# Kernel optimization log

Hardware: AMD Instinct MI355X
Metric: run time of the kernel (lower is better)

Reference implementation:

```python
import jax, jax.numpy as jnp
import numpy as np

DIM = 768
HEADS = 12
HD = DIM // HEADS
B, NX, NY = 8, 1024, 1024
GRID = 32
FREQ = 100.0
MLP_HID = 4 * DIM
EPS = 1e-5


def _grid_pos(batch, n, grid):
    g = int(np.sqrt(n))
    yy, xx = jnp.meshgrid(jnp.arange(g, dtype=jnp.int32), jnp.arange(g, dtype=jnp.int32), indexing='ij')
    pos = jnp.stack([yy.reshape(-1), xx.reshape(-1)], axis=-1)  # [N,2]
    return jnp.broadcast_to(pos[None], (batch, n, 2))


def setup_inputs() -> dict:
    key = jax.random.key(0)
    ks = jax.random.split(key, 16)
    s = 0.02
    inp = {
        'x': jax.random.normal(ks[0], (B, NX, DIM), jnp.float32),
        'y': jax.random.normal(ks[1], (B, NY, DIM), jnp.float32),
        'xpos': _grid_pos(B, NX, GRID),
        'ypos': _grid_pos(B, NY, GRID),
        # norms (gamma, beta)
        'norm1_g': jnp.ones((DIM,), jnp.float32), 'norm1_b': jnp.zeros((DIM,), jnp.float32),
        'norm2_g': jnp.ones((DIM,), jnp.float32), 'norm2_b': jnp.zeros((DIM,), jnp.float32),
        'norm3_g': jnp.ones((DIM,), jnp.float32), 'norm3_b': jnp.zeros((DIM,), jnp.float32),
        'normy_g': jnp.ones((DIM,), jnp.float32), 'normy_b': jnp.zeros((DIM,), jnp.float32),
        # self-attn: fused qkv (no bias, qkv_bias=False), out proj (with bias)
        'qkv_w': jax.random.normal(ks[2], (DIM, 3 * DIM), jnp.float32) * s,
        'attn_proj_w': jax.random.normal(ks[3], (DIM, DIM), jnp.float32) * s,
        'attn_proj_b': jnp.zeros((DIM,), jnp.float32),
        # cross-attn: separate q/k/v (no bias), out proj (with bias)
        'projq_w': jax.random.normal(ks[4], (DIM, DIM), jnp.float32) * s,
        'projk_w': jax.random.normal(ks[5], (DIM, DIM), jnp.float32) * s,
        'projv_w': jax.random.normal(ks[6], (DIM, DIM), jnp.float32) * s,
        'cross_proj_w': jax.random.normal(ks[7], (DIM, DIM), jnp.float32) * s,
        'cross_proj_b': jnp.zeros((DIM,), jnp.float32),
        # MLP
        'fc1_w': jax.random.normal(ks[8], (DIM, MLP_HID), jnp.float32) * s,
        'fc1_b': jnp.zeros((MLP_HID,), jnp.float32),
        'fc2_w': jax.random.normal(ks[9], (MLP_HID, DIM), jnp.float32) * s,
        'fc2_b': jnp.zeros((DIM,), jnp.float32),
    }
    return inp


def layernorm(x, g, b):
    m = jnp.mean(x, axis=-1, keepdims=True)
    v = jnp.mean(jnp.square(x - m), axis=-1, keepdims=True)
    return (x - m) * jax.lax.rsqrt(v + EPS) * g + b


def rope1d(tok, pos):
    # tok: [B,H,N,D], pos: [B,N] int
    D = tok.shape[-1]
    inv = 1.0 / (FREQ ** (jnp.arange(0, D, 2, dtype=jnp.float32) / D))  # [D/2]
    f = pos[:, None, :, None].astype(jnp.float32) * inv  # [B,1,N,D/2]
    emb = jnp.concatenate([f, f], axis=-1)  # [B,1,N,D]
    cos, sin = jnp.cos(emb), jnp.sin(emb)
    t1, t2 = jnp.split(tok, 2, axis=-1)
    rot = jnp.concatenate([-t2, t1], axis=-1)
    return tok * cos + rot * sin


def rope2d(tok, pos):
    # first half of head dim rotated by y-coord, second half by x-coord
    ty, tx = jnp.split(tok, 2, axis=-1)
    return jnp.concatenate([rope1d(ty, pos[..., 0]), rope1d(tx, pos[..., 1])], axis=-1)


def sdpa(q, k, v):
    scale = q.shape[-1] ** -0.5
    a = jax.nn.softmax(jnp.einsum('bhqd,bhkd->bhqk', q, k) * scale, axis=-1)
    return jnp.einsum('bhqk,bhkd->bhqd', a, v)


def split_heads(t):  # [B,N,C] -> [B,H,N,HD]
    Bv, N, C = t.shape
    return t.reshape(Bv, N, HEADS, HD).transpose(0, 2, 1, 3)


def merge_heads(t):  # [B,H,N,HD] -> [B,N,C]
    Bv, H, N, D = t.shape
    return t.transpose(0, 2, 1, 3).reshape(Bv, N, H * D)


def reference(x, y, xpos, ypos,
              norm1_g, norm1_b, norm2_g, norm2_b, norm3_g, norm3_b, normy_g, normy_b,
              qkv_w, attn_proj_w, attn_proj_b,
              projq_w, projk_w, projv_w, cross_proj_w, cross_proj_b,
              fc1_w, fc1_b, fc2_w, fc2_b):
    # --- self attention ---
    h = layernorm(x, norm1_g, norm1_b)
    qkv = h @ qkv_w  # [B,N,3C]
    q, k, v = (split_heads(t) for t in jnp.split(qkv, 3, axis=-1))
    q = rope2d(q, xpos)
    k = rope2d(k, xpos)
    x = x + merge_heads(sdpa(q, k, v)) @ attn_proj_w + attn_proj_b

    # --- cross attention ---
    y_ = layernorm(y, normy_g, normy_b)
    hq = layernorm(x, norm2_g, norm2_b)
    q = rope2d(split_heads(hq @ projq_w), xpos)
    k = rope2d(split_heads(y_ @ projk_w), ypos)
    v = split_heads(y_ @ projv_w)
    x = x + merge_heads(sdpa(q, k, v)) @ cross_proj_w + cross_proj_b

    # --- MLP ---
    h = layernorm(x, norm3_g, norm3_b)
    x = x + jax.nn.gelu(h @ fc1_w + fc1_b, approximate=False) @ fc2_w + fc2_b
    return (x, y)
```

## Files before the change

kernel.cpp:

```cpp
#include <hip/hip_runtime.h>
#include <hip/hip_bf16.h>
#include <math.h>

#define DIM 768
#define HEADS 12
#define HD 64
#define BB 8
#define NN 1024
#define EPSV 1e-5f

typedef unsigned int uint32;
typedef unsigned short ushort_t;
using short8 = __attribute__((ext_vector_type(8))) short;
using f32x4 = __attribute__((ext_vector_type(4))) float;

static __device__ inline ushort_t f2b(float v) {
    uint32 u = __float_as_uint(v);
    return (ushort_t)((u + 0x7FFFu + ((u >> 16) & 1u)) >> 16);
}
static __device__ inline float b2f(ushort_t v) {
    return __uint_as_float((uint32)v << 16);
}

static __device__ inline float erf_fast(float x) {
    float ax = fabsf(x);
    float t = __frcp_rn(1.0f + 0.3275911f * ax);
    float p = t * (0.254829592f + t * (-0.284496736f + t * (1.421413741f +
              t * (-1.453152027f + t * 1.061405429f))));
    float e = 1.0f - p * __expf(-ax * ax);
    return copysignf(e, x);
}

static __device__ __forceinline__ void gload_lds16(const ushort_t* g, ushort_t* l) {
    __builtin_amdgcn_global_load_lds(
        (const __attribute__((address_space(1))) void*)g,
        (__attribute__((address_space(3))) void*)l, 16, 0, 0);
}

__global__ __launch_bounds__(256) void ln_bf16(const float* __restrict__ in,
                                               const float* __restrict__ g,
                                               const float* __restrict__ b,
                                               ushort_t* __restrict__ out) {
    int r = blockIdx.x;
    const float* x = in + (size_t)r * DIM;
    ushort_t* o = out + (size_t)r * DIM;
    int t = threadIdx.x;
    float v0 = x[t], v1 = x[t + 256], v2 = x[t + 512];
    float s = v0 + v1 + v2;
    float s2 = v0 * v0 + v1 * v1 + v2 * v2;
    for (int off = 32; off; off >>= 1) {
        s += __shfl_xor(s, off);
        s2 += __shfl_xor(s2, off);
    }
    __shared__ float ls[4], lq[4];
    int wid = t >> 6;
    if ((t & 63) == 0) { ls[wid] = s; lq[wid] = s2; }
    __syncthreads();
    s = ls[0] + ls[1] + ls[2] + ls[3];
    s2 = lq[0] + lq[1] + lq[2] + lq[3];
    float mean = s * (1.0f / DIM);
    float var = s2 * (1.0f / DIM) - mean * mean;
    float rs = rsqrtf(var + EPSV);
    o[t]       = f2b((v0 - mean) * rs * g[t]       + b[t]);
    o[t + 256] = f2b((v1 - mean) * rs * g[t + 256] + b[t + 256]);
    o[t + 512] = f2b((v2 - mean) * rs * g[t + 512] + b[t + 512]);
}

struct XArgs {
    const float* src[8];
    ushort_t* dst[8];
    int K[8], N[8];
    int tstart[9];
};
__global__ __launch_bounds__(256) void xform_w(XArgs a) {
    __shared__ float tl[32][33];
    int t = blockIdx.x;
    int w = 0;
    while (t >= a.tstart[w + 1]) w++;
    int lt = t - a.tstart[w];
    int ntn = a.N[w] >> 5;
    int k0 = (lt / ntn) * 32, n0 = (lt % ntn) * 32;
    const float* src = a.src[w];
    ushort_t* dst = a.dst[w];
    int K = a.K[w], N = a.N[w];
    int rr = threadIdx.x >> 5, cc = threadIdx.x & 31;
#pragma unroll
    for (int u = 0; u < 4; u++)
        tl[rr + u * 8][cc] = src[(size_t)(k0 + rr + u * 8) * N + n0 + cc];
    __syncthreads();
#pragma unroll
    for (int u = 0; u < 4; u++)
        dst[(size_t)(n0 + rr + u * 8) * K + k0 + cc] = f2b(tl[cc][rr + u * 8]);
}

template <int ACT, int OBF16>
__global__ __launch_bounds__(256) void gemm_mfma(const ushort_t* __restrict__ A,
                                                 const ushort_t* __restrict__ Wt,
                                                 const float* __restrict__ bias,
                                                 const float* res,
                                                 void* Cout, int M, int N, int K) {
    __shared__ ushort_t As[2][128 * 64];
    __shared__ ushort_t Bs[2][128 * 64];
    int nblk = N >> 7;
    int nwg = (M >> 7) * nblk;
    int bid = blockIdx.x;
    int wg = (bid & 7) * (nwg >> 3) + (bid >> 3);
    int bx = wg % nblk, by = wg / nblk;
    int m0 = by * 128, n0 = bx * 128;
    int tid = threadIdx.x;
    int wid = tid >> 6, lane = tid & 63;
    int wm = wid >> 1, wn = wid & 1;
    int l15 = lane & 15, lh = lane >> 4;

    int srow0 = wid * 32 + (lane >> 3);
    int cslot = lane & 7;

    auto STAGE = [&](int buf, int k0) {
#pragma unroll
        for (int inst = 0; inst < 4; inst++) {
            int r = srow0 + inst * 8;
            int csrc = (cslot ^ (r & 7)) << 3;
            gload_lds16(A + (size_t)(m0 + r) * K + k0 + csrc,
                        &As[buf][(wid * 4 + inst) * 512]);
            gload_lds16(Wt + (size_t)(n0 + r) * K + k0 + csrc,
                        &Bs[buf][(wid * 4 + inst) * 512]);
        }
    };

    STAGE(0, 0);
    f32x4 acc[4][4] = {};
    __syncthreads();

    int nT = K >> 6;
    int cur = 0;
    for (int t = 0; t < nT; t++) {
        if (t + 1 < nT) STAGE(cur ^ 1, (t + 1) << 6);
#pragma unroll
        for (int ks8 = 0; ks8 < 2; ks8++) {
            int cA = ks8 * 4 + lh;
            short8 af[4], bfr[4];
#pragma unroll
            for (int i = 0; i < 4; i++) {
                int rA = wm * 64 + i * 16 + l15;
                af[i] = *(const short8*)&As[cur][rA * 64 + ((cA ^ (rA & 7)) << 3)];
                int rB = wn * 64 + i * 16 + l15;
                bfr[i] = *(const short8*)&Bs[cur][rB * 64 + ((cA ^ (rB & 7)) << 3)];
            }
#pragma unroll
            for (int i = 0; i < 4; i++)
#pragma unroll
                for (int j = 0; j < 4; j++)
                    acc[i][j] = __builtin_amdgcn_mfma_f32_16x16x32_bf16(
                        af[i], bfr[j], acc[i][j], 0, 0, 0);
        }
        __syncthreads();
        cur ^= 1;
    }

    __syncthreads();
    float* ep = (float*)&As[0][0] + wid * (16 * 68);
    int erow = lane >> 2, ecol = (lane & 3) * 16;
#pragma unroll
    for (int i = 0; i < 4; i++) {
#pragma unroll
        for (int j = 0; j < 4; j++) {
            int n = n0 + wn * 64 + j * 16 + l15;
            float bv = bias ? bias[n] : 0.0f;
#pragma unroll
            for (int r = 0; r < 4; r++) {
                float v = acc[i][j][r] + bv;
                if (ACT == 1) v = 0.5f * v * (1.0f + erf_fast(v * 0.70710678118654752f));
                ep[(lh * 4 + r) * 68 + j * 16 + l15] = v;
            }
        }
        int m = m0 + wm * 64 + i * 16 + erow;
        size_t off = (size_t)m * N + n0 + wn * 64 + ecol;
        float vv[16];
#pragma unroll
        for (int u = 0; u < 4; u++)
            *(float4*)&vv[u * 4] = *(float4*)&ep[erow * 68 + ecol + u * 4];
        if (res) {
#pragma unroll
            for (int u = 0; u < 4; u++) {
                float4 rv = *(const float4*)(res + off + u * 4);
                vv[u * 4 + 0] += rv.x;
                vv[u * 4 + 1] += rv.y;
                vv[u * 4 + 2] += rv.z;
                vv[u * 4 + 3] += rv.w;
            }
        }
        if (OBF16) {
            ushort_t tb[16];
#pragma unroll
            for (int u = 0; u < 16; u++) tb[u] = f2b(vv[u]);
            *(uint4*)((ushort_t*)Cout + off)     = *(uint4*)&tb[0];
            *(uint4*)((ushort_t*)Cout + off + 8) = *(uint4*)&tb[8];
        } else {
#pragma unroll
            for (int u = 0; u < 4; u++)
                *(float4*)((float*)Cout + off + u * 4) = *(float4*)&vv[u * 4];
        }
    }
}

__global__ __launch_bounds__(256) void rope2_bf16(ushort_t* __restrict__ ta,
                                                  const int* __restrict__ pa, int sa,
                                                  ushort_t* __restrict__ tb,
                                                  const int* __restrict__ pb, int sb,
                                                  int rt) {
    int idx = blockIdx.x * 256 + threadIdx.x;
    ushort_t* t;
    const int* pos;
    int rowStride;
    if (idx >= rt) { idx -= rt; t = tb; pos = pb; rowStride = sb; }
    else           { t = ta; pos = pa; rowStride = sa; }
    int i = idx & 15;
    int half = (idx >> 4) & 1;
    int h = (idx >> 5) % HEADS;
    int bn = idx / (HEADS * 32);
    int p = pos[(size_t)bn * 2 + half];
    float inv = powf(100.0f, -(float)i / 16.0f);
    float f = (float)p * inv;
    float c, s;
    sincosf(f, &s, &c);
    ushort_t* base = t + (size_t)bn * rowStride + h * HD + half * 32;
    float t1 = b2f(base[i]), t2 = b2f(base[i + 16]);
    base[i]      = f2b(t1 * c - t2 * s);
    base[i + 16] = f2b(t2 * c + t1 * s);
}

__global__ __launch_bounds__(256) void transpose_v(const ushort_t* __restrict__ src,
                                                   int ss, ushort_t* __restrict__ dst) {
    __shared__ ushort_t tl[64][66];
    int bid = blockIdx.x;
    int nt = bid & 15;
    int h = (bid >> 4) % HEADS;
    int b = bid / (16 * HEADS);
    int n0 = nt * 64;
    int t = threadIdx.x;
    int r = t >> 2, c0 = (t & 3) * 16;
    const ushort_t* s = src + ((size_t)(b * NN) + n0 + r) * ss + h * HD + c0;
    *(uint4*)&tl[r][c0]     = *(const uint4*)s;
    *(uint4*)&tl[r][c0 + 8] = *(const uint4*)(s + 8);
    __syncthreads();
    ushort_t* d = dst + (((size_t)(b * HEADS + h)) * HD + r) * NN + n0 + c0;
    ushort_t tmp[16];
#pragma unroll
    for (int u = 0; u < 16; u++) tmp[u] = tl[c0 + u][r];
    *(uint4*)d       = *(uint4*)tmp;
    *(uint4*)(d + 8) = *(uint4*)(tmp + 8);
}

__global__ __launch_bounds__(256) void attn_mfma(const ushort_t* __restrict__ Q, int sq,
                                                 const ushort_t* __restrict__ K, int sk,
                                                 const ushort_t* __restrict__ VT,
                                                 ushort_t* __restrict__ O, int so) {
    __shared__ ushort_t Qs[64][72];
    __shared__ ushort_t Ks[64][72];
    __shared__ ushort_t Vs[64][72];
    __shared__ ushort_t Ps[64][72];

    int bid = blockIdx.x;
    int qb = bid & 15;
    int h = (bid >> 4) % HEADS;
    int b = bid / (16 * HEADS);
    int n0 = qb * 64;

    int tid = threadIdx.x;
    int lane = tid & 63, wq = tid >> 6;
    int l15 = lane & 15, lh = lane >> 4;

    const ushort_t* Qbase = Q + (size_t)b * NN * sq + h * HD;
    const ushort_t* Kbase = K + (size_t)b * NN * sk + h * HD;
    const ushort_t* VTbase = VT + ((size_t)(b * HEADS + h)) * HD * NN;
    ushort_t* Obase = O + (size_t)b * NN * so + h * HD;

    int row = tid >> 2, c0 = (tid & 3) * 16;
    {
        const ushort_t* src = Qbase + (size_t)(n0 + row) * sq + c0;
        *(uint4*)&Qs[row][c0]     = *(const uint4*)src;
        *(uint4*)&Qs[row][c0 + 8] = *(const uint4*)(src + 8);
    }

    const ushort_t* kp = Kbase + (size_t)row * sk + c0;
    const ushort_t* vp = VTbase + (size_t)row * NN + c0;
    uint4 rk0 = *(const uint4*)kp, rk1 = *(const uint4*)(kp + 8);
    uint4 rv0 = *(const uint4*)vp, rv1 = *(const uint4*)(vp + 8);

    f32x4 oacc[4] = {};
    float mrow[4] = {-1e30f, -1e30f, -1e30f, -1e30f};
    float lrow[4] = {};

    for (int kt = 0; kt < NN / 64; kt++) {
        __syncthreads();
        *(uint4*)&Ks[row][c0]     = rk0;
        *(uint4*)&Ks[row][c0 + 8] = rk1;
        *(uint4*)&Vs[row][c0]     = rv0;
        *(uint4*)&Vs[row][c0 + 8] = rv1;
        __syncthreads();
        if (kt + 1 < NN / 64) {
            const ushort_t* kp2 = kp + (size_t)(kt + 1) * 64 * sk;
            const ushort_t* vp2 = vp + (size_t)(kt + 1) * 64;
            rk0 = *(const uint4*)kp2;
            rk1 = *(const uint4*)(kp2 + 8);
            rv0 = *(const uint4*)vp2;
            rv1 = *(const uint4*)(vp2 + 8);
        }

        f32x4 s[4] = {};
#pragma unroll
        for (int ks8 = 0; ks8 < 2; ks8++) {
            short8 aq = *(const short8*)&Qs[wq * 16 + l15][ks8 * 32 + lh * 8];
#pragma unroll
            for (int j = 0; j < 4; j++) {
                short8 bk = *(const short8*)&Ks[j * 16 + l15][ks8 * 32 + lh * 8];
                s[j] = __builtin_amdgcn_mfma_f32_16x16x32_bf16(aq, bk, s[j], 0, 0, 0);
            }
        }

        float corr[4];
#pragma unroll
        for (int r = 0; r < 4; r++) {
            float v0 = s[0][r] * 0.125f, v1 = s[1][r] * 0.125f;
            float v2 = s[2][r] * 0.125f, v3 = s[3][r] * 0.125f;
            float rm = fmaxf(fmaxf(v0, v1), fmaxf(v2, v3));
            rm = fmaxf(rm, __shfl_xor(rm, 1));
            rm = fmaxf(rm, __shfl_xor(rm, 2));
            rm = fmaxf(rm, __shfl_xor(rm, 4));
            rm = fmaxf(rm, __shfl_xor(rm, 8));
            float mn = fmaxf(mrow[r], rm);
            corr[r] = __expf(mrow[r] - mn);
            mrow[r] = mn;
            float p0 = __expf(v0 - mn), p1 = __expf(v1 - mn);
            float p2 = __expf(v2 - mn), p3 = __expf(v3 - mn);
            float ps = p0 + p1 + p2 + p3;
            ps += __shfl_xor(ps, 1);
            ps += __shfl_xor(ps, 2);
            ps += __shfl_xor(ps, 4);
            ps += __shfl_xor(ps, 8);
            lrow[r] = lrow[r] * corr[r] + ps;
            int qrow = wq * 16 + lh * 4 + r;
            Ps[qrow][0 * 16 + l15] = f2b(p0);
            Ps[qrow][1 * 16 + l15] = f2b(p1);
            Ps[qrow][2 * 16 + l15] = f2b(p2);
            Ps[qrow][3 * 16 + l15] = f2b(p3);
        }
#pragma unroll
        for (int j = 0; j < 4; j++)
#pragma unroll
            for (int r = 0; r < 4; r++) oacc[j][r] *= corr[r];

#pragma unroll
        for (int ks8 = 0; ks8 < 2; ks8++) {
            short8 ap = *(const short8*)&Ps[wq * 16 + l15][ks8 * 32 + lh * 8];
#pragma unroll
            for (int j = 0; j < 4; j++) {
                short8 bv = *(const short8*)&Vs[j * 16 + l15][ks8 * 32 + lh * 8];
                oacc[j] = __builtin_amdgcn_mfma_f32_16x16x32_bf16(ap, bv, oacc[j], 0, 0, 0);
            }
        }
    }

#pragma unroll
    for (int r = 0; r < 4; r++) {
        float inv = 1.0f / lrow[r];
        int prow = wq * 16 + lh * 4 + r;
#pragma unroll
        for (int j = 0; j < 4; j++)
            Ps[prow][j * 16 + l15] = f2b(oacc[j][r] * inv);
    }
    int erow = lane >> 2, ecol = (lane & 3) * 16;
    uint4 w0 = *(uint4*)&Ps[wq * 16 + erow][ecol];
    uint4 w1 = *(uint4*)&Ps[wq * 16 + erow][ecol + 8];
    ushort_t* op = Obase + (size_t)(n0 + wq * 16 + erow) * so + ecol;
    *(uint4*)op       = w0;
    *(uint4*)(op + 8) = w1;
}

__global__ __launch_bounds__(256) void fill_f32(float* __restrict__ out, float v, int n) {
    int i = blockIdx.x * 256 + threadIdx.x;
    if (i < n) out[i] = v;
}

extern "C" void kernel_launch(void* const* d_in, const int* in_sizes, int n_in,
                              void* d_out, int out_size, void* d_ws, size_t ws_size,
                              hipStream_t stream) {
    const float* x = (const float*)d_in[0];
    const float* y = (const float*)d_in[1];
    const int* xpos = (const int*)d_in[2];
    const int* ypos = (const int*)d_in[3];
    const float* norm1_g = (const float*)d_in[4];
    const float* norm1_b = (const float*)d_in[5];
    const float* norm2_g = (const float*)d_in[6];
    const float* norm2_b = (const float*)d_in[7];
    const float* norm3_g = (const float*)d_in[8];
    const float* norm3_b = (const float*)d_in[9];
    const float* normy_g = (const float*)d_in[10];
    const float* normy_b = (const float*)d_in[11];
    const float* qkv_w = (const float*)d_in[12];
    const float* attn_proj_w = (const float*)d_in[13];
    const float* attn_proj_b = (const float*)d_in[14];
    const float* projq_w = (const float*)d_in[15];
    const float* projk_w = (const float*)d_in[16];
    const float* projv_w = (const float*)d_in[17];
    const float* cross_proj_w = (const float*)d_in[18];
    const float* cross_proj_b = (const float*)d_in[19];
    const float* fc1_w = (const float*)d_in[20];
    const float* fc1_b = (const float*)d_in[21];
    const float* fc2_w = (const float*)d_in[22];
    const float* fc2_b = (const float*)d_in[23];
    float* out = (float*)d_out;

    const size_t SZ = (size_t)BB * NN * DIM;
    const int ROWS = BB * NN;

    const size_t WS_NEED = SZ * 4 + SZ * 2 + 4 * SZ * 2 + 9437184ull * 2;

    {
        const int expect[24] = {
            (int)SZ, (int)SZ, BB * NN * 2, BB * NN * 2,
            DIM, DIM, DIM, DIM, DIM, DIM, DIM, DIM,
            DIM * 3 * DIM, DIM * DIM, DIM,
            DIM * DIM, DIM * DIM, DIM * DIM, DIM * DIM, DIM,
            DIM * 4 * DIM, 4 * DIM, 4 * DIM * DIM, DIM};
        float sentinel = 0.0f;
        if (n_in != 24) sentinel = 2000.0f;
        else {
            for (int i = 0; i < 24; i++)
                if (in_sizes[i] != expect[i]) { sentinel = 1000.0f + i; break; }
        }
        if (sentinel == 0.0f && ws_size < WS_NEED) sentinel = 3000.0f;
        if (sentinel == 0.0f && out_size != (int)(2 * SZ)) sentinel = 4000.0f;
        if (sentinel != 0.0f) {
            fill_f32<<<(int)((SZ + 255) / 256), 256, 0, stream>>>(out, sentinel, (int)SZ);
            return;
        }
    }

    float* bufX = (float*)d_ws;
    ushort_t* bufAb = (ushort_t*)(bufX + SZ);
    ushort_t* bufQKVb = bufAb + SZ;
    ushort_t* wts = bufQKVb + 4 * SZ;

    ushort_t* qkvT = wts;
    ushort_t* apT  = qkvT + 2304 * 768;
    ushort_t* pqT  = apT + 768 * 768;
    ushort_t* pkT  = pqT + 768 * 768;
    ushort_t* pvT  = pkT + 768 * 768;
    ushort_t* cpT  = pvT + 768 * 768;
    ushort_t* fc1T = cpT + 768 * 768;
    ushort_t* fc2T = fc1T + 3072 * 768;
    ushort_t* HID  = bufQKVb;

    XArgs xa;
    xa.src[0] = qkv_w;        xa.dst[0] = qkvT; xa.K[0] = 768;  xa.N[0] = 2304;
    xa.src[1] = attn_proj_w;  xa.dst[1] = apT;  xa.K[1] = 768;  xa.N[1] = 768;
    xa.src[2] = projq_w;      xa.dst[2] = pqT;  xa.K[2] = 768;  xa.N[2] = 768;
    xa.src[3] = projk_w;      xa.dst[3] = pkT;  xa.K[3] = 768;  xa.N[3] = 768;
    xa.src[4] = projv_w;      xa.dst[4] = pvT;  xa.K[4] = 768;  xa.N[4] = 768;
    xa.src[5] = cross_proj_w; xa.dst[5] = cpT;  xa.K[5] = 768;  xa.N[5] = 768;
    xa.src[6] = fc1_w;        xa.dst[6] = fc1T; xa.K[6] = 768;  xa.N[6] = 3072;
    xa.src[7] = fc2_w;        xa.dst[7] = fc2T; xa.K[7] = 3072; xa.N[7] = 768;
    int acc_t = 0;
    for (int i = 0; i < 8; i++) {
        xa.tstart[i] = acc_t;
        acc_t += (xa.K[i] / 32) * (xa.N[i] / 32);
    }
    xa.tstart[8] = acc_t;
    xform_w<<<acc_t, 256, 0, stream>>>(xa);

    const int rt = ROWS * HEADS * 32;
    const int attnGrid = BB * HEADS * (NN / 64);
    ushort_t* VTg;

    ln_bf16<<<ROWS, 256, 0, stream>>>(x, norm1_g, norm1_b, bufAb);
    gemm_mfma<0, 1><<<64 * 18, 256, 0, stream>>>(bufAb, qkvT, nullptr, nullptr,
                                                 bufQKVb, ROWS, 2304, 768);
    rope2_bf16<<<2 * rt / 256, 256, 0, stream>>>(bufQKVb, xpos, 2304,
                                                 bufQKVb + DIM, xpos, 2304, rt);
    VTg = bufQKVb + 3 * SZ;
    transpose_v<<<attnGrid, 256, 0, stream>>>(bufQKVb + 2 * DIM, 2304, VTg);
    attn_mfma<<<attnGrid, 256, 0, stream>>>(bufQKVb, 2304, bufQKVb + DIM, 2304,
                                            VTg, bufAb, DIM);
    gemm_mfma<0, 0><<<64 * 6, 256, 0, stream>>>(bufAb, apT, attn_proj_b, x,
                                                bufX, ROWS, 768, 768);

    ushort_t* Qc = bufQKVb;
    ushort_t* KVc = bufQKVb + SZ;
    ln_bf16<<<ROWS, 256, 0, stream>>>(bufX, norm2_g, norm2_b, bufAb);
    gemm_mfma<0, 1><<<64 * 6, 256, 0, stream>>>(bufAb, pqT, nullptr, nullptr,
                                                Qc, ROWS, 768, 768);
    ln_bf16<<<ROWS, 256, 0, stream>>>(y, normy_g, normy_b, bufAb);
    gemm_mfma<0, 1><<<64 * 12, 256, 0, stream>>>(bufAb, pkT, nullptr, nullptr,
                                                 KVc, ROWS, 1536, 768);
    rope2_bf16<<<2 * rt / 256, 256, 0, stream>>>(Qc, xpos, 768,
                                                 KVc, ypos, 1536, rt);
    VTg = bufQKVb + 3 * SZ;
    transpose_v<<<attnGrid, 256, 0, stream>>>(KVc + DIM, 1536, VTg);
    attn_mfma<<<attnGrid, 256, 0, stream>>>(Qc, 768, KVc, 1536, VTg, bufAb, DIM);
    gemm_mfma<0, 0><<<64 * 6, 256, 0, stream>>>(bufAb, cpT, cross_proj_b, bufX,
                                                bufX, ROWS, 768, 768);

    ln_bf16<<<ROWS, 256, 0, stream>>>(bufX, norm3_g, norm3_b, bufAb);
    gemm_mfma<1, 1><<<64 * 24, 256, 0, stream>>>(bufAb, fc1T, fc1_b, nullptr,
                                                 HID, ROWS, 3072, 768);
    gemm_mfma<0, 0><<<64 * 6, 256, 0, stream>>>(HID, fc2T, fc2_b, bufX,
                                                out, ROWS, 768, 3072);

    hipMemcpyAsync(out + SZ, y, SZ * sizeof(float), hipMemcpyDeviceToDevice, stream);
}
```

Before: 537.2 us.

## Halve GEMM K-tile to 32 and remap workgroups per XCD to row blocks

The bf16 MFMA GEMM now stages 128x32 K-slices instead of 128x64, which halves the double-buffered LDS footprint and changes the XOR swizzle to a 4-slot pattern. Each loop iteration now issues one k-step of MFMAs instead of two. Workgroup IDs are remapped so each XCD owns a contiguous group of 8 row blocks and loops over column blocks, aiming for better L2 reuse of A rows. The lower LDS use may allow more resident workgroups, at the cost of twice as many barriers and less latency hiding per stage. The new mapping hardcodes M/128 = 64.

Result: slower. 560.5 us (+4.3%).

```diff
diff --git a/kernel.cpp b/kernel.cpp
--- a/kernel.cpp
+++ b/kernel.cpp
@@ -99,31 +99,28 @@
                                                  const float* __restrict__ bias,
                                                  const float* res,
                                                  void* Cout, int M, int N, int K) {
-    __shared__ ushort_t As[2][128 * 64];
-    __shared__ ushort_t Bs[2][128 * 64];
-    int nblk = N >> 7;
-    int nwg = (M >> 7) * nblk;
+    __shared__ ushort_t lds[4][128 * 32];
     int bid = blockIdx.x;
-    int wg = (bid & 7) * (nwg >> 3) + (bid >> 3);
-    int bx = wg % nblk, by = wg / nblk;
+    int xcd = bid & 7, rr = bid >> 3;
+    int bx = rr >> 3;
+    int by = xcd * 8 + (rr & 7);
     int m0 = by * 128, n0 = bx * 128;
     int tid = threadIdx.x;
     int wid = tid >> 6, lane = tid & 63;
     int wm = wid >> 1, wn = wid & 1;
     int l15 = lane & 15, lh = lane >> 4;
 
-    int srow0 = wid * 32 + (lane >> 3);
-    int cslot = lane & 7;
+    int srow = lane >> 2, cslot = lane & 3;
 
     auto STAGE = [&](int buf, int k0) {
 #pragma unroll
-        for (int inst = 0; inst < 4; inst++) {
-            int r = srow0 + inst * 8;
-            int csrc = (cslot ^ (r & 7)) << 3;
-            gload_lds16(A + (size_t)(m0 + r) * K + k0 + csrc,
-                        &As[buf][(wid * 4 + inst) * 512]);
-            gload_lds16(Wt + (size_t)(n0 + r) * K + k0 + csrc,
-                        &Bs[buf][(wid * 4 + inst) * 512]);
+        for (int inst = 0; inst < 2; inst++) {
+            int r0 = (wid * 2 + inst) * 16 + srow;
+            int csrc = (cslot ^ (r0 & 3)) << 3;
+            gload_lds16(A + (size_t)(m0 + r0) * K + k0 + csrc,
+                        &lds[buf * 2 + 0][(wid * 2 + inst) * 512]);
+            gload_lds16(Wt + (size_t)(n0 + r0) * K + k0 + csrc,
+                        &lds[buf * 2 + 1][(wid * 2 + inst) * 512]);
         }
     };
 
@@ -131,34 +128,29 @@
     f32x4 acc[4][4] = {};
     __syncthreads();
 
-    int nT = K >> 6;
+    int nT = K >> 5;
     int cur = 0;
     for (int t = 0; t < nT; t++) {
-        if (t + 1 < nT) STAGE(cur ^ 1, (t + 1) << 6);
-#pragma unroll
-        for (int ks8 = 0; ks8 < 2; ks8++) {
-            int cA = ks8 * 4 + lh;
-            short8 af[4], bfr[4];
-#pragma unroll
-            for (int i = 0; i < 4; i++) {
-                int rA = wm * 64 + i * 16 + l15;
-                af[i] = *(const short8*)&As[cur][rA * 64 + ((cA ^ (rA & 7)) << 3)];
-                int rB = wn * 64 + i * 16 + l15;
-                bfr[i] = *(const short8*)&Bs[cur][rB * 64 + ((cA ^ (rB & 7)) << 3)];
-            }
-#pragma unroll
-            for (int i = 0; i < 4; i++)
-#pragma unroll
-                for (int j = 0; j < 4; j++)
-                    acc[i][j] = __builtin_amdgcn_mfma_f32_16x16x32_bf16(
-                        af[i], bfr[j], acc[i][j], 0, 0, 0);
-        }
+        if (t + 1 < nT) STAGE(cur ^ 1, (t + 1) << 5);
+        short8 af[4], bfr[4];
+#pragma unroll
+        for (int i = 0; i < 4; i++) {
+            int rA = wm * 64 + i * 16 + l15;
+            af[i] = *(const short8*)&lds[cur * 2 + 0][rA * 32 + ((lh ^ (rA & 3)) << 3)];
+            int rB = wn * 64 + i * 16 + l15;
+            bfr[i] = *(const short8*)&lds[cur * 2 + 1][rB * 32 + ((lh ^ (rB & 3)) << 3)];
+        }
+#pragma unroll
+        for (int i = 0; i < 4; i++)
+#pragma unroll
+            for (int j = 0; j < 4; j++)
+                acc[i][j] = __builtin_amdgcn_mfma_f32_16x16x32_bf16(
+                    af[i], bfr[j], acc[i][j], 0, 0, 0);
         __syncthreads();
         cur ^= 1;
     }
 
-    __syncthreads();
-    float* ep = (float*)&As[0][0] + wid * (16 * 68);
+    float* ep = (float*)&lds[0][0] + wid * 1088;
     int erow = lane >> 2, ecol = (lane & 3) * 16;
 #pragma unroll
     for (int i = 0; i < 4; i++) {
```
